# Performance work log

Hardware: AMD Instinct MI355X
Metric: run time of the kernel (lower is better)

The kernel has to match this reference:

```python
import jax, jax.numpy as jnp
import numpy as np


def conv2d(x, w, b, stride=1, pad=1):
    y = jax.lax.conv_general_dilated(
        x, w, (stride, stride), [(pad, pad), (pad, pad)],
        dimension_numbers=('NCHW', 'OIHW', 'NCHW'))
    return y + b[None, :, None, None]


def layernorm(x, g, b, eps=1e-5):
    mu = jnp.mean(x, -1, keepdims=True)
    var = jnp.mean((x - mu) ** 2, -1, keepdims=True)
    return (x - mu) * jax.lax.rsqrt(var + eps) * g + b


def setup_inputs() -> dict:
    key = jax.random.key(0)
    ks = iter(jax.random.split(key, 40))
    nf = 4

    def w(shape, scale=0.1):
        return (jax.random.normal(next(ks), shape, jnp.float32) * scale)

    inp = {}
    inp['x'] = jax.random.uniform(next(ks), (8, 3, 512, 512), jnp.float32)
    # curve-estimation convs (channel=4)
    inp['c1_w'], inp['c1_b'] = w((nf, 1, 3, 3)), w((nf,))
    inp['c2_w'], inp['c2_b'] = w((nf, nf, 3, 3)), w((nf,))
    inp['c3_w'], inp['c3_b'] = w((nf, nf, 3, 3)), w((nf,))
    inp['c4_w'], inp['c4_b'] = w((nf, nf, 3, 3)), w((nf,))
    inp['c5_w'], inp['c5_b'] = w((nf, 2 * nf, 3, 3)), w((nf,))
    inp['c6_w'], inp['c6_b'] = w((nf, 2 * nf, 3, 3)), w((nf,))
    inp['c7_w'], inp['c7_b'] = w((1, 2 * nf, 3, 3)), w((1,))
    # global branch: conv 1->16 stride 2, instance norm (affine)
    inp['m_w'], inp['m_b'] = w((16, 1, 3, 3)), w((16,))
    inp['in_g'] = jnp.ones((16,), jnp.float32)
    inp['in_b'] = jnp.zeros((16,), jnp.float32)
    # TF block (d_model=16, nhead=8, dim_ff=128), eval mode (no dropout)
    inp['attn_w'], inp['attn_b'] = w((48, 16)), w((48,))
    inp['out_w'], inp['out_b'] = w((16, 16)), w((16,))
    inp['l1_w'], inp['l1_b'] = w((128, 16)), w((128,))
    inp['l2_w'], inp['l2_b'] = w((16, 128)), w((16,))
    inp['n1_g'] = jnp.ones((16,), jnp.float32)
    inp['n1_b'] = jnp.zeros((16,), jnp.float32)
    inp['n2_g'] = jnp.ones((16,), jnp.float32)
    inp['n2_b'] = jnp.zeros((16,), jnp.float32)
    # F: Conv2d(16, 2, kernel=16, pad=0) over 16x16 -> [B,2,1,1]
    inp['f_w'], inp['f_b'] = w((2, 16, 16, 16)), w((2,))
    return inp


def _forward(x, c1_w, c1_b, c2_w, c2_b, c3_w, c3_b, c4_w, c4_b, c5_w, c5_b,
             c6_w, c6_b, c7_w, c7_b, m_w, m_b, in_g, in_b, attn_w, attn_b,
             out_w, out_b, l1_w, l1_b, l2_w, l2_b, n1_g, n1_b, n2_g, n2_b,
             f_w, f_b):
    relu = jax.nn.relu
    B, _, H, W = x.shape
    red, green, blue = x[:, 0:1], x[:, 1:2], x[:, 2:3]
    v = (red + green + blue) / 3.0  # [B,1,H,W]

    # curve-estimation branch
    x1 = relu(conv2d(v, c1_w, c1_b))
    x2 = relu(conv2d(x1, c2_w, c2_b))
    x3 = relu(conv2d(x2, c3_w, c3_b))
    x4 = relu(conv2d(x3, c4_w, c4_b))
    x5 = relu(conv2d(jnp.concatenate([x3, x4], 1), c5_w, c5_b))
    x6 = relu(conv2d(jnp.concatenate([x2, x5], 1), c6_w, c6_b))
    v_r = jax.nn.sigmoid(conv2d(jnp.concatenate([x1, x6], 1), c7_w, c7_b))

    # where(v>0.999999, 0.999999, .) ; where(v<1e-6, 1e-6, .)  == clip
    v0 = jnp.clip(v, 1e-6, 0.999999)

    # nearest-neighbor resize to 32x32 (torch 'nearest': floor(i * src/dst))
    idx_h = (jnp.arange(32) * H) // 32
    idx_w = (jnp.arange(32) * W) // 32
    v32 = v[:, :, idx_h][:, :, :, idx_w]  # [B,1,32,32]

    # model: conv stride2 -> leaky relu -> instance norm (affine)
    h = conv2d(v32, m_w, m_b, stride=2, pad=1)  # [B,16,16,16]
    h = jnp.where(h >= 0, h, 0.2 * h)
    mu = jnp.mean(h, (2, 3), keepdims=True)
    var = jnp.mean((h - mu) ** 2, (2, 3), keepdims=True)
    v1 = (h - mu) * jax.lax.rsqrt(var + 1e-5)
    v1 = v1 * in_g[None, :, None, None] + in_b[None, :, None, None]

    # TF block on [S=256, B, E=16] tokens, 8 heads of dim 2, eval mode
    bb, cc, ww, hh = v1.shape
    src = v1.reshape(bb, cc, ww * hh).transpose(2, 0, 1)  # [S,B,E]
    S, E, nH = ww * hh, cc, 8
    hd = E // nH
    qkv = src @ attn_w.T + attn_b  # [S,B,3E]
    q, k, vv = jnp.split(qkv, 3, axis=-1)
    q = q.reshape(S, bb, nH, hd)
    k = k.reshape(S, bb, nH, hd)
    vv = vv.reshape(S, bb, nH, hd)
    scores = jnp.einsum('sbhd,tbhd->bhst', q, k) / np.sqrt(hd).astype(np.float32)
    attn = jax.nn.softmax(scores, axis=-1)
    o = jnp.einsum('bhst,tbhd->sbhd', attn, vv).reshape(S, bb, E)
    o = o @ out_w.T + out_b
    src = layernorm(src + o, n1_g, n1_b)
    ff = jax.nn.relu(src @ l1_w.T + l1_b) @ l2_w.T + l2_b
    src = layernorm(src + ff, n2_g, n2_b)
    v5 = src.transpose(1, 2, 0).reshape(bb, cc, ww, hh)

    level = jax.nn.sigmoid(conv2d(v5, f_w, f_b, stride=1, pad=0))[:, :, 0, 0]  # [B,2]

    # per-sample exponent / threshold broadcast (vectorized .item() loop)
    g = (0.1 * level[:, 0] + 0.2)[:, None, None, None]   # [B,1,1,1]
    bcf = (0.04 * level[:, 1] + 0.06)[:, None, None, None]
    r0 = jnp.power(g, v_r)           # g ** r, elementwise per sample
    ev0 = jnp.power(v0, r0)
    L = 400.0 * (bcf - v) ** 3
    L = jnp.where(L < 1e-5, 1e-6, L)
    ev = ev0 - L
    vd = v + 1e-6
    enhance = jnp.concatenate([red / vd * ev, green / vd * ev, blue / vd * ev], 1)
    vvv = jnp.concatenate([v, v, v], 1)
    t = jnp.where(vvv > 0.04, jnp.zeros_like(enhance), enhance)
    return enhance, v_r, t


def reference(x, c1_w, c1_b, c2_w, c2_b, c3_w, c3_b, c4_w, c4_b, c5_w, c5_b,
              c6_w, c6_b, c7_w, c7_b, m_w, m_b, in_g, in_b, attn_w, attn_b,
              out_w, out_b, l1_w, l1_b, l2_w, l2_b, n1_g, n1_b, n2_g, n2_b,
              f_w, f_b):
    return _forward(x, c1_w, c1_b, c2_w, c2_b, c3_w, c3_b, c4_w, c4_b,
                    c5_w, c5_b, c6_w, c6_b, c7_w, c7_b, m_w, m_b, in_g, in_b,
                    attn_w, attn_b, out_w, out_b, l1_w, l1_b, l2_w, l2_b,
                    n1_g, n1_b, n2_g, n2_b, f_w, f_b)
```

## Files before the change

kernel.cpp:

```cpp
#include <hip/hip_runtime.h>
#include <math.h>

#define H 512
#define W 512
#define PLANE (H*W)
#define PLANE4 (PLANE/4)

typedef unsigned int uint;
typedef unsigned short ushort;
typedef _Float16 h2 __attribute__((ext_vector_type(2)));

__device__ __forceinline__ h2 bch2(uint u){ return __builtin_bit_cast(h2, u); }
__device__ __forceinline__ uint pkf16(float a, float b){
  return __builtin_bit_cast(uint, __builtin_amdgcn_cvt_pkrtz(a, b));
}

#define LOADWIN_EVEN(WIN, TL, S, YB, XB) { \
  _Pragma("unroll") for (int r_=0;r_<4;++r_){ \
    uint4 Ua = *(const uint4*)&(TL)[(((YB)+r_)*(S)+(XB))*4]; \
    uint4 Ub = *(const uint4*)&(TL)[(((YB)+r_)*(S)+(XB)+2)*4]; \
    WIN[r_][0][0]=bch2(Ua.x); WIN[r_][0][1]=bch2(Ua.y); \
    WIN[r_][1][0]=bch2(Ua.z); WIN[r_][1][1]=bch2(Ua.w); \
    WIN[r_][2][0]=bch2(Ub.x); WIN[r_][2][1]=bch2(Ub.y); \
    WIN[r_][3][0]=bch2(Ub.z); WIN[r_][3][1]=bch2(Ub.w); } }

#define LOADWIN_ODD(WIN, TL, S, YB, XB) { \
  _Pragma("unroll") for (int r_=0;r_<4;++r_){ \
    uint2 U0 = *(const uint2*)&(TL)[(((YB)+r_)*(S)+(XB))*4]; \
    uint4 U1 = *(const uint4*)&(TL)[(((YB)+r_)*(S)+(XB)+1)*4]; \
    uint2 U2 = *(const uint2*)&(TL)[(((YB)+r_)*(S)+(XB)+3)*4]; \
    WIN[r_][0][0]=bch2(U0.x); WIN[r_][0][1]=bch2(U0.y); \
    WIN[r_][1][0]=bch2(U1.x); WIN[r_][1][1]=bch2(U1.y); \
    WIN[r_][2][0]=bch2(U1.z); WIN[r_][2][1]=bch2(U1.w); \
    WIN[r_][3][0]=bch2(U2.x); WIN[r_][3][1]=bch2(U2.y); } }

#define LOADW(WL, OFF) uint WL[72]; \
  _Pragma("unroll") for (int i_=0;i_<72;++i_) WL[i_] = wpk[(OFF)+i_];

#define DOTACC2(WIN, WL) { \
  _Pragma("unroll") for (int p_=0;p_<2;++p_){ \
    _Pragma("unroll") for (int dy_=0;dy_<3;++dy_){ \
      _Pragma("unroll") for (int dx_=0;dx_<3;++dx_){ \
        h2 aa=WIN[dy_][dx_][p_],   bb=WIN[dy_][dx_+1][p_]; \
        h2 cc=WIN[dy_+1][dx_][p_], dd=WIN[dy_+1][dx_+1][p_]; \
        _Pragma("unroll") for (int co_=0;co_<4;++co_){ \
          h2 wv = bch2((WL)[(co_*2+p_)*9+dy_*3+dx_]); \
          a00[co_]=__builtin_amdgcn_fdot2(aa,wv,a00[co_],false); \
          a01[co_]=__builtin_amdgcn_fdot2(bb,wv,a01[co_],false); \
          a10[co_]=__builtin_amdgcn_fdot2(cc,wv,a10[co_],false); \
          a11[co_]=__builtin_amdgcn_fdot2(dd,wv,a11[co_],false); } } } } }

#define DOTACC1(WIN, WL, PBASE) { \
  _Pragma("unroll") for (int p_=0;p_<2;++p_){ \
    _Pragma("unroll") for (int dy_=0;dy_<3;++dy_){ \
      _Pragma("unroll") for (int dx_=0;dx_<3;++dx_){ \
        h2 wv = bch2((WL)[((PBASE)+p_)*9+dy_*3+dx_]); \
        s00=__builtin_amdgcn_fdot2(WIN[dy_][dx_][p_],  wv,s00,false); \
        s01=__builtin_amdgcn_fdot2(WIN[dy_][dx_+1][p_],wv,s01,false); \
        s10=__builtin_amdgcn_fdot2(WIN[dy_+1][dx_][p_],  wv,s10,false); \
        s11=__builtin_amdgcn_fdot2(WIN[dy_+1][dx_+1][p_],wv,s11,false); } } } }

#define STORE_CORE(TL, S, M00, M01, M10, M11) { \
    float v00[4],v01[4],v10[4],v11[4]; \
    _Pragma("unroll") \
    for (int co_=0;co_<4;++co_){ \
      v00[co_]=(M00)?fmaxf(a00[co_],0.f):0.f; \
      v01[co_]=(M01)?fmaxf(a01[co_],0.f):0.f; \
      v10[co_]=(M10)?fmaxf(a10[co_],0.f):0.f; \
      v11[co_]=(M11)?fmaxf(a11[co_],0.f):0.f; } \
    uint4 rowlo, rowhi; \
    rowlo.x=pkf16(v00[0],v00[1]); rowlo.y=pkf16(v00[2],v00[3]); \
    rowlo.z=pkf16(v01[0],v01[1]); rowlo.w=pkf16(v01[2],v01[3]); \
    rowhi.x=pkf16(v10[0],v10[1]); rowhi.y=pkf16(v10[2],v10[3]); \
    rowhi.z=pkf16(v11[0],v11[1]); rowhi.w=pkf16(v11[2],v11[3]); \
    *(uint4*)&(TL)[(y0*(S)+x0)*4]=rowlo; \
    *(uint4*)&(TL)[((y0+1)*(S)+x0)*4]=rowhi; }

#define STORE_TILE_B(TL, S, GOFF) { \
    bool okr0=(unsigned)(gy0+(GOFF)+y0  )<512u; \
    bool okr1=(unsigned)(gy0+(GOFF)+y0+1)<512u; \
    bool okc0=(unsigned)(gx0+(GOFF)+x0  )<512u; \
    bool okc1=(unsigned)(gx0+(GOFF)+x0+1)<512u; \
    STORE_CORE(TL, S, okr0&okc0, okr0&okc1, okr1&okc0, okr1&okc1) }

template<int S>
__device__ __forceinline__ void accp4sc(const ushort* __restrict__ pl,
    const float* __restrict__ w, int YB, int XB,
    float* a00, float* a01, float* a10, float* a11)
{
  float q[4][4];
  #pragma unroll
  for (int r=0;r<4;++r){
    const ushort* rp = pl + (YB+r)*S + XB;
    h2 p0 = bch2(*(const uint*)rp);
    h2 p1 = bch2(*(const uint*)(rp+2));
    q[r][0]=(float)p0.x; q[r][1]=(float)p0.y; q[r][2]=(float)p1.x; q[r][3]=(float)p1.y;
  }
  #pragma unroll
  for (int dy=0; dy<3; ++dy)
    #pragma unroll
    for (int dx=0; dx<3; ++dx){
      float q00=q[dy][dx], q01=q[dy][dx+1], q10=q[dy+1][dx], q11=q[dy+1][dx+1];
      #pragma unroll
      for (int co=0; co<4; ++co){
        float wv=w[co*9+dy*3+dx];
        a00[co]+=q00*wv; a01[co]+=q01*wv; a10[co]+=q10*wv; a11[co]+=q11*wv;
      }
    }
}

__launch_bounds__(256)
__global__ void k_mnorm(const float* __restrict__ xg, const float* __restrict__ mw,
                        const float* __restrict__ mb, const float* __restrict__ ing,
                        const float* __restrict__ inb, float* __restrict__ src,
                        const float* __restrict__ c2w, const float* __restrict__ c3w,
                        const float* __restrict__ c4w, const float* __restrict__ c5w,
                        const float* __restrict__ c6w, const float* __restrict__ c7w,
                        uint* __restrict__ wpk){
  if (blockIdx.x == 128){
    for (int i=threadIdx.x; i<540; i+=256){
      float f0, f1;
      if (i < 504){
        const float* sw; int CIB, rel;
        if      (i<72) { sw=c2w; CIB=0; rel=i;     int co=rel/18,p=(rel%18)/9,tap=rel%9;
                         f0=sw[(co*4+CIB+2*p)*9+tap]; f1=sw[(co*4+CIB+2*p+1)*9+tap]; }
        else if (i<144){ sw=c3w; CIB=0; rel=i-72;  int co=rel/18,p=(rel%18)/9,tap=rel%9;
                         f0=sw[(co*4+CIB+2*p)*9+tap]; f1=sw[(co*4+CIB+2*p+1)*9+tap]; }
        else if (i<216){ sw=c4w; CIB=0; rel=i-144; int co=rel/18,p=(rel%18)/9,tap=rel%9;
                         f0=sw[(co*4+CIB+2*p)*9+tap]; f1=sw[(co*4+CIB+2*p+1)*9+tap]; }
        else if (i<288){ sw=c5w; CIB=0; rel=i-216; int co=rel/18,p=(rel%18)/9,tap=rel%9;
                         f0=sw[(co*8+CIB+2*p)*9+tap]; f1=sw[(co*8+CIB+2*p+1)*9+tap]; }
        else if (i<360){ sw=c5w; CIB=4; rel=i-288; int co=rel/18,p=(rel%18)/9,tap=rel%9;
                         f0=sw[(co*8+CIB+2*p)*9+tap]; f1=sw[(co*8+CIB+2*p+1)*9+tap]; }
        else if (i<432){ sw=c6w; CIB=0; rel=i-360; int co=rel/18,p=(rel%18)/9,tap=rel%9;
                         f0=sw[(co*8+CIB+2*p)*9+tap]; f1=sw[(co*8+CIB+2*p+1)*9+tap]; }
        else           { sw=c6w; CIB=4; rel=i-432; int co=rel/18,p=(rel%18)/9,tap=rel%9;
                         f0=sw[(co*8+CIB+2*p)*9+tap]; f1=sw[(co*8+CIB+2*p+1)*9+tap]; }
      } else {
        int rel=i-504, p=rel/9, tap=rel%9;
        f0=c7w[(2*p)*9+tap]; f1=c7w[(2*p+1)*9+tap];
      }
      wpk[i] = pkf16(f0, f1);
    }
    return;
  }
  int bc = blockIdx.x;
  int b = bc >> 4, c = bc & 15;
  int tid = threadIdx.x;
  int i = tid >> 4, j = tid & 15;
  const float* xp = xg + (size_t)b*3*PLANE;
  float s = mb[c];
  #pragma unroll
  for (int dy=0; dy<3; ++dy){
    int ii = 2*i - 1 + dy;
    if ((unsigned)ii >= 32u) continue;
    #pragma unroll
    for (int dx=0; dx<3; ++dx){
      int jj = 2*j - 1 + dx;
      if ((unsigned)jj >= 32u) continue;
      int off = (ii*16)*W + jj*16;
      float vv = (xp[off] + xp[PLANE+off] + xp[2*PLANE+off]) * (1.f/3.f);
      s += vv * mw[c*9 + dy*3 + dx];
    }
  }
  float h = (s >= 0.f) ? s : 0.2f*s;
  __shared__ float red[256];
  red[tid] = h; __syncthreads();
  for (int off=128; off; off>>=1){ if (tid<off) red[tid]+=red[tid+off]; __syncthreads(); }
  float mu = red[0] * (1.f/256.f);
  __syncthreads();
  float d = h - mu;
  red[tid] = d*d; __syncthreads();
  for (int off=128; off; off>>=1){ if (tid<off) red[tid]+=red[tid+off]; __syncthreads(); }
  float var = red[0] * (1.f/256.f);
  float yv = d * rsqrtf(var + 1e-5f) * ing[c] + inb[c];
  src[(size_t)tid*128 + b*16 + c] = yv;
}

__launch_bounds__(256)
__global__ void k_attn2(const float* __restrict__ src, const float* __restrict__ aw,
                        const float* __restrict__ ab, float* __restrict__ obuf){
  int b = blockIdx.x >> 3, hh = blockIdx.x & 7;
  int t = threadIdx.x;
  __shared__ float kk0[256], kk1[256], vv0[256], vv1[256];
  int tok = t*8 + b;
  float s[16];
  #pragma unroll
  for (int e=0;e<16;++e) s[e] = src[tok*16+e];
  float q0=ab[2*hh], q1=ab[2*hh+1];
  float k0=ab[16+2*hh], k1=ab[16+2*hh+1];
  float v0=ab[32+2*hh], v1=ab[32+2*hh+1];
  #pragma unroll
  for (int e=0;e<16;++e){
    float sv=s[e];
    q0 += sv*aw[(2*hh  )*16+e]; q1 += sv*aw[(2*hh+1)*16+e];
    k0 += sv*aw[(16+2*hh)*16+e]; k1 += sv*aw[(16+2*hh+1)*16+e];
    v0 += sv*aw[(32+2*hh)*16+e]; v1 += sv*aw[(32+2*hh+1)*16+e];
  }
  kk0[t]=k0; kk1[t]=k1; vv0[t]=v0; vv1[t]=v1;
  __syncthreads();
  const float sc = 0.70710678118654752f;
  float l=0.f, a0=0.f, a1=0.f;
  for (int u=0;u<256;++u){
    float p = __expf((q0*kk0[u]+q1*kk1[u])*sc);
    l+=p; a0+=p*vv0[u]; a1+=p*vv1[u];
  }
  float inv=1.f/l;
  obuf[tok*16 + 2*hh]   = a0*inv;
  obuf[tok*16 + 2*hh+1] = a1*inv;
}

__launch_bounds__(256)
__global__ void k_post(const float* __restrict__ src, const float* __restrict__ obuf,
                       const float* __restrict__ ow, const float* __restrict__ ob,
                       const float* __restrict__ l1w, const float* __restrict__ l1b,
                       const float* __restrict__ l2w, const float* __restrict__ l2b,
                       const float* __restrict__ n1g, const float* __restrict__ n1b,
                       const float* __restrict__ n2g, const float* __restrict__ n2b,
                       const float* __restrict__ fw, const float* __restrict__ fb,
                       float* __restrict__ gb){
  __shared__ float srcl[256][17];
  __shared__ float red[512];
  int b = blockIdx.x, t = threadIdx.x;
  int tok = t*8 + b;
  float xv[16];
  {
    float orow[16], srow[16];
    #pragma unroll
    for (int e=0;e<16;++e){ orow[e]=obuf[tok*16+e]; srow[e]=src[tok*16+e]; }
    #pragma unroll
    for (int e=0;e<16;++e){
      float s2=ob[e];
      #pragma unroll
      for (int f=0;f<16;++f) s2 += orow[f]*ow[e*16+f];
      xv[e]=srow[e]+s2;
    }
    float mu=0.f;
    #pragma unroll
    for (int e=0;e<16;++e) mu+=xv[e];
    mu*=(1.f/16.f);
    float var=0.f;
    #pragma unroll
    for (int e=0;e<16;++e){ float d=xv[e]-mu; var+=d*d; }
    var*=(1.f/16.f);
    float rs=rsqrtf(var+1e-5f);
    #pragma unroll
    for (int e=0;e<16;++e) xv[e]=(xv[e]-mu)*rs*n1g[e]+n1b[e];
  }
  {
    float x2[16];
    #pragma unroll
    for (int e=0;e<16;++e) x2[e]=l2b[e];
    for (int ii=0;ii<128;++ii){
      float u=l1b[ii];
      #pragma unroll
      for (int e=0;e<16;++e) u += xv[e]*l1w[ii*16+e];
      u = fmaxf(u,0.f);
      #pragma unroll
      for (int e=0;e<16;++e) x2[e] += u*l2w[e*128+ii];
    }
    #pragma unroll
    for (int e=0;e<16;++e) x2[e]+=xv[e];
    float mu=0.f;
    #pragma unroll
    for (int e=0;e<16;++e) mu+=x2[e];
    mu*=(1.f/16.f);
    float var=0.f;
    #pragma unroll
    for (int e=0;e<16;++e){ float d=x2[e]-mu; var+=d*d; }
    var*=(1.f/16.f);
    float rs=rsqrtf(var+1e-5f);
    #pragma unroll
    for (int e=0;e<16;++e) srcl[t][e]=(x2[e]-mu)*rs*n2g[e]+n2b[e];
  }
  __syncthreads();
  {
    float p0=0.f,p1=0.f;
    #pragma unroll
    for (int c=0;c<16;++c){
      float sv=srcl[t][c];
      p0 += sv*fw[c*256+t];
      p1 += sv*fw[(16+c)*256+t];
    }
    red[t]=p0; red[256+t]=p1;
  }
  __syncthreads();
  for (int off=128; off; off>>=1){
    if (t<off){ red[t]+=red[t+off]; red[256+t]+=red[256+t+off]; }
    __syncthreads();
  }
  if (t==0){
    float lev0 = 1.f/(1.f+__expf(-(red[0]+fb[0])));
    float lev1 = 1.f/(1.f+__expf(-(red[256]+fb[1])));
    gb[b*2+0] = 0.1f*lev0+0.2f;
    gb[b*2+1] = 0.04f*lev1+0.06f;
  }
}

__launch_bounds__(512,2)
__global__ void k_megaconv(const float* __restrict__ xg,
    const float* __restrict__ c1w, const float* __restrict__ c1b,
    const float* __restrict__ c2b, const float* __restrict__ c3b,
    const float* __restrict__ c4b, const float* __restrict__ c5b,
    const float* __restrict__ c6b, const float* __restrict__ c7b,
    const uint* __restrict__ wpk, const float* __restrict__ gb2,
    float* __restrict__ out)
{
  __shared__ __align__(16) ushort vb[46*46];
  __shared__ __align__(16) ushort t1[44*44*4];
  __shared__ __align__(16) ushort t2[42*42*4];
  __shared__ __align__(16) ushort t3[40*40*4];
  __shared__ __align__(16) ushort t4[38*38*4];
  __shared__ __align__(16) ushort t5[36*36*4];
  __shared__ __align__(16) ushort t6[34*34*4];
  int wg=blockIdx.x, b=wg>>8, t=wg&255, ty=t>>4, tx=t&15;
  int gy0=ty*32, gx0=tx*32, tid=threadIdx.x;
  const float* xp = xg + (size_t)b*3*PLANE;
  const bool interior = (ty>=1)&(ty<=14)&(tx>=1)&(tx<=14);

  if (interior){
    for (int i=tid;i<46*46;i+=512){
      int rr=i/46, cc=i-rr*46;
      int off=(gy0-7+rr)*W + gx0-7+cc;
      float val=(xp[off]+xp[PLANE+off]+xp[2*PLANE+off])*(1.f/3.f);
      _Float16 hv=(_Float16)val;
      vb[i]=*(ushort*)&hv;
    }
  } else {
    for (int i=tid;i<46*46;i+=512){
      int rr=i/46, cc=i-rr*46;
      int gy=gy0-7+rr, gx=gx0-7+cc;
      float val=0.f;
      if (((unsigned)gy<512u)&((unsigned)gx<512u)){
        int off=gy*W+gx;
        val=(xp[off]+xp[PLANE+off]+xp[2*PLANE+off])*(1.f/3.f);
      }
      _Float16 hv=(_Float16)val;
      vb[i]=*(ushort*)&hv;
    }
  }
  __syncthreads();

  if (tid < 484){
    int qy=tid/22, qx=tid-qy*22, y0=2*qy, x0=2*qx;
    float a00[4],a01[4],a10[4],a11[4];
    #pragma unroll
    for (int co=0;co<4;++co){ float bv=c1b[co]; a00[co]=bv;a01[co]=bv;a10[co]=bv;a11[co]=bv; }
    accp4sc<46>(vb, c1w, y0, x0, a00,a01,a10,a11);
    if (interior){ STORE_CORE(t1, 44, true, true, true, true) }
    else         { STORE_TILE_B(t1, 44, -6) }
  }
  __syncthreads();

  if (tid < 441){
    int qy=tid/21, qx=tid-qy*21, y0=2*qy, x0=2*qx;
    float a00[4],a01[4],a10[4],a11[4];
    #pragma unroll
    for (int co=0;co<4;++co){ float bv=c2b[co]; a00[co]=bv;a01[co]=bv;a10[co]=bv;a11[co]=bv; }
    h2 win[4][4][2];
    LOADWIN_EVEN(win, t1, 44, y0, x0)
    LOADW(wl2, 0)
    DOTACC2(win, wl2)
    if (interior){ STORE_CORE(t2, 42, true, true, true, true) }
    else         { STORE_TILE_B(t2, 42, -5) }
  }
  __syncthreads();

  if (tid < 400){
    int qy=tid/20, qx=tid-qy*20, y0=2*qy, x0=2*qx;
    float a00[4],a01[4],a10[4],a11[4];
    #pragma unroll
    for (int co=0;co<4;++co){ float bv=c3b[co]; a00[co]=bv;a01[co]=bv;a10[co]=bv;a11[co]=bv; }
    h2 win[4][4][2];
    LOADWIN_EVEN(win, t2, 42, y0, x0)
    LOADW(wl3, 72)
    DOTACC2(win, wl3)
    if (interior){ STORE_CORE(t3, 40, true, true, true, true) }
    else         { STORE_TILE_B(t3, 40, -4) }
  }
  __syncthreads();

  if (tid < 361){
    int qy=tid/19, qx=tid-qy*19, y0=2*qy, x0=2*qx;
    float a00[4],a01[4],a10[4],a11[4];
    #pragma unroll
    for (int co=0;co<4;++co){ float bv=c4b[co]; a00[co]=bv;a01[co]=bv;a10[co]=bv;a11[co]=bv; }
    h2 win[4][4][2];
    LOADWIN_EVEN(win, t3, 40, y0, x0)
    LOADW(wl4, 144)
    DOTACC2(win, wl4)
    if (interior){ STORE_CORE(t4, 38, true, true, true, true) }
    else         { STORE_TILE_B(t4, 38, -3) }
  }
  __syncthreads();

  if (tid < 324){
    int qy=tid/18, qx=tid-qy*18, y0=2*qy, x0=2*qx;
    float a00[4],a01[4],a10[4],a11[4];
    #pragma unroll
    for (int co=0;co<4;++co){ float bv=c5b[co]; a00[co]=bv;a01[co]=bv;a10[co]=bv;a11[co]=bv; }
    {
      h2 win[4][4][2];
      LOADWIN_ODD(win, t3, 40, y0+1, x0+1)
      LOADW(wlA, 216)
      DOTACC2(win, wlA)
    }
    {
      h2 win[4][4][2];
      LOADWIN_EVEN(win, t4, 38, y0, x0)
      LOADW(wlB, 288)
      DOTACC2(win, wlB)
    }
    if (interior){ STORE_CORE(t5, 36, true, true, true, true) }
    else         { STORE_TILE_B(t5, 36, -2) }
  }
  __syncthreads();

  if (tid < 289){
    int qy=tid/17, qx=tid-qy*17, y0=2*qy, x0=2*qx;
    float a00[4],a01[4],a10[4],a11[4];
    #pragma unroll
    for (int co=0;co<4;++co){ float bv=c6b[co]; a00[co]=bv;a01[co]=bv;a10[co]=bv;a11[co]=bv; }
    {
      h2 win[4][4][2];
      LOADWIN_ODD(win, t2, 42, y0+3, x0+3)
      LOADW(wlA, 360)
      DOTACC2(win, wlA)
    }
    {
      h2 win[4][4][2];
      LOADWIN_EVEN(win, t5, 36, y0, x0)
      LOADW(wlB, 432)
      DOTACC2(win, wlB)
    }
    if (interior){ STORE_CORE(t6, 34, true, true, true, true) }
    else         { STORE_TILE_B(t6, 34, -1) }
  }
  __syncthreads();

  if (tid < 256){
    int qy=tid>>4, qx=tid&15, y0=2*qy, x0=2*qx;
    float bv=c7b[0];
    float s00=bv, s01=bv, s10=bv, s11=bv;
    uint wl7[36];
    #pragma unroll
    for (int i_=0;i_<36;++i_) wl7[i_]=wpk[504+i_];
    {
      h2 win[4][4][2];
      LOADWIN_ODD(win, t1, 44, y0+5, x0+5)
      DOTACC1(win, wl7, 0)
    }
    {
      h2 win[4][4][2];
      LOADWIN_EVEN(win, t6, 34, y0, x0)
      DOTACC1(win, wl7, 2)
    }
    s00 = 1.f/(1.f+__expf(-s00)); s01 = 1.f/(1.f+__expf(-s01));
    s10 = 1.f/(1.f+__expf(-s10)); s11 = 1.f/(1.f+__expf(-s11));
    float* vo = out + 6291456 + (size_t)b*PLANE;
    *(float2*)&vo[(gy0+y0  )*512 + gx0+x0] = make_float2(s00,s01);
    *(float2*)&vo[(gy0+y0+1)*512 + gx0+x0] = make_float2(s10,s11);

    float gg = gb2[b*2+0], bcf = gb2[b*2+1];
    float lg = log2f(gg);
    #pragma unroll
    for (int py=0; py<2; ++py){
      int gy=gy0+y0+py, gx=gx0+x0;
      int off=gy*W+gx;
      float2 R = *(const float2*)&xp[off];
      float2 G = *(const float2*)&xp[PLANE+off];
      float2 B = *(const float2*)&xp[2*PLANE+off];
      float vr0 = py? s10:s00, vr1 = py? s11:s01;
      float2 er,eg,eb,tr,tg,tb;
#define COMP1(RF,GF,BF,VRF,ER,EG,EB,TR,TG,TB) { \
      float vv=(RF+GF+BF)*(1.f/3.f); \
      float v0c=fminf(fmaxf(vv,1e-6f),0.999999f); \
      float r0=exp2f((VRF)*lg); \
      float ev0=exp2f(r0*log2f(v0c)); \
      float dd=bcf-vv; \
      float L=400.f*dd*dd*dd; \
      L=(L<1e-5f)?1e-6f:L; \
      float fac=(ev0-L)/(vv+1e-6f); \
      ER=RF*fac; EG=GF*fac; EB=BF*fac; \
      bool z=vv>0.04f; \
      TR=z?0.f:ER; TG=z?0.f:EG; TB=z?0.f:EB; }
      COMP1(R.x,G.x,B.x,vr0, er.x,eg.x,eb.x, tr.x,tg.x,tb.x)
      COMP1(R.y,G.y,B.y,vr1, er.y,eg.y,eb.y, tr.y,tg.y,tb.y)
#undef COMP1
      *(float2*)&out[(size_t)(b*3+0)*PLANE + off] = er;
      *(float2*)&out[(size_t)(b*3+1)*PLANE + off] = eg;
      *(float2*)&out[(size_t)(b*3+2)*PLANE + off] = eb;
      *(float2*)&out[8388608 + (size_t)(b*3+0)*PLANE + off] = tr;
      *(float2*)&out[8388608 + (size_t)(b*3+1)*PLANE + off] = tg;
      *(float2*)&out[8388608 + (size_t)(b*3+2)*PLANE + off] = tb;
    }
  }
}

extern "C" void kernel_launch(void* const* d_in, const int* in_sizes, int n_in,
                              void* d_out, int out_size, void* d_ws, size_t ws_size,
                              hipStream_t stream) {
  const float* x    = (const float*)d_in[0];
  const float* c1w  = (const float*)d_in[1];  const float* c1b = (const float*)d_in[2];
  const float* c2w  = (const float*)d_in[3];  const float* c2b = (const float*)d_in[4];
  const float* c3w  = (const float*)d_in[5];  const float* c3b = (const float*)d_in[6];
  const float* c4w  = (const float*)d_in[7];  const float* c4b = (const float*)d_in[8];
  const float* c5w  = (const float*)d_in[9];  const float* c5b = (const float*)d_in[10];
  const float* c6w  = (const float*)d_in[11]; const float* c6b = (const float*)d_in[12];
  const float* c7w  = (const float*)d_in[13]; const float* c7b = (const float*)d_in[14];
  const float* mw   = (const float*)d_in[15]; const float* mb  = (const float*)d_in[16];
  const float* ing  = (const float*)d_in[17]; const float* inb = (const float*)d_in[18];
  const float* aw   = (const float*)d_in[19]; const float* ab  = (const float*)d_in[20];
  const float* ow   = (const float*)d_in[21]; const float* ob  = (const float*)d_in[22];
  const float* l1w  = (const float*)d_in[23]; const float* l1b = (const float*)d_in[24];
  const float* l2w  = (const float*)d_in[25]; const float* l2b = (const float*)d_in[26];
  const float* n1g  = (const float*)d_in[27]; const float* n1b = (const float*)d_in[28];
  const float* n2g  = (const float*)d_in[29]; const float* n2b = (const float*)d_in[30];
  const float* fw   = (const float*)d_in[31]; const float* fb  = (const float*)d_in[32];

  uint* wpk = (uint*)d_ws;
  float* gb   = (float*)(wpk + 1024);
  float* src  = gb + 16;
  float* obuf = src + 32768;
  float* out  = (float*)d_out;

  k_mnorm<<<129,256,0,stream>>>(x, mw, mb, ing, inb, src,
                                c2w, c3w, c4w, c5w, c6w, c7w, wpk);
  k_attn2<<<64,256,0,stream>>>(src, aw, ab, obuf);
  k_post<<<8,256,0,stream>>>(src, obuf, ow, ob, l1w, l1b, l2w, l2b,
                             n1g, n1b, n2g, n2b, fw, fb, gb);
  k_megaconv<<<2048,512,0,stream>>>(x, c1w, c1b, c2b, c3b, c4b, c5b, c6b, c7b,
                                    wpk, gb, out);
}
```

Measured before the change: 184.1 us.

## Parallelize transformer post-processing per token with atomic accumulation into gate buffer

Result: faster. 153.7 us (median of 3 runs) (-16.5%).

```diff
diff --git a/kernel.cpp b/kernel.cpp
--- a/kernel.cpp
+++ b/kernel.cpp
@@ -116,8 +116,9 @@
                         const float* __restrict__ c2w, const float* __restrict__ c3w,
                         const float* __restrict__ c4w, const float* __restrict__ c5w,
                         const float* __restrict__ c6w, const float* __restrict__ c7w,
-                        uint* __restrict__ wpk){
+                        uint* __restrict__ wpk, float* __restrict__ gbacc){
   if (blockIdx.x == 128){
+    if (threadIdx.x < 16) gbacc[threadIdx.x] = 0.f;
     for (int i=threadIdx.x; i<540; i+=256){
       float f0, f1;
       if (i < 504){
@@ -210,90 +211,66 @@
   obuf[tok*16 + 2*hh+1] = a1*inv;
 }
 
-__launch_bounds__(256)
-__global__ void k_post(const float* __restrict__ src, const float* __restrict__ obuf,
-                       const float* __restrict__ ow, const float* __restrict__ ob,
-                       const float* __restrict__ l1w, const float* __restrict__ l1b,
-                       const float* __restrict__ l2w, const float* __restrict__ l2b,
-                       const float* __restrict__ n1g, const float* __restrict__ n1b,
-                       const float* __restrict__ n2g, const float* __restrict__ n2b,
-                       const float* __restrict__ fw, const float* __restrict__ fb,
-                       float* __restrict__ gb){
-  __shared__ float srcl[256][17];
-  __shared__ float red[512];
-  int b = blockIdx.x, t = threadIdx.x;
-  int tok = t*8 + b;
-  float xv[16];
-  {
-    float orow[16], srow[16];
-    #pragma unroll
-    for (int e=0;e<16;++e){ orow[e]=obuf[tok*16+e]; srow[e]=src[tok*16+e]; }
-    #pragma unroll
-    for (int e=0;e<16;++e){
-      float s2=ob[e];
-      #pragma unroll
-      for (int f=0;f<16;++f) s2 += orow[f]*ow[e*16+f];
-      xv[e]=srow[e]+s2;
-    }
+__launch_bounds__(64)
+__global__ void k_tok(const float* __restrict__ src, const float* __restrict__ obuf,
+                      const float* __restrict__ ow, const float* __restrict__ ob,
+                      const float* __restrict__ l1w, const float* __restrict__ l1b,
+                      const float* __restrict__ l2w, const float* __restrict__ l2b,
+                      const float* __restrict__ n1g, const float* __restrict__ n1b,
+                      const float* __restrict__ n2g, const float* __restrict__ n2b,
+                      const float* __restrict__ fw, float* __restrict__ gbacc){
+  int tok = blockIdx.x, tid = threadIdx.x;
+  int s = tok >> 3, b = tok & 7;
+  __shared__ float shx[16], shy[16], h1[128];
+  if (tid < 16){
+    float t2 = ob[tid];
+    #pragma unroll
+    for (int f=0;f<16;++f) t2 += obuf[tok*16+f]*ow[tid*16+f];
+    shx[tid] = src[tok*16+tid] + t2;
+  }
+  __syncthreads();
+  if (tid < 16){
     float mu=0.f;
     #pragma unroll
-    for (int e=0;e<16;++e) mu+=xv[e];
+    for (int e=0;e<16;++e) mu+=shx[e];
     mu*=(1.f/16.f);
     float var=0.f;
     #pragma unroll
-    for (int e=0;e<16;++e){ float d=xv[e]-mu; var+=d*d; }
+    for (int e=0;e<16;++e){ float d=shx[e]-mu; var+=d*d; }
     var*=(1.f/16.f);
-    float rs=rsqrtf(var+1e-5f);
-    #pragma unroll
-    for (int e=0;e<16;++e) xv[e]=(xv[e]-mu)*rs*n1g[e]+n1b[e];
-  }
-  {
-    float x2[16];
-    #pragma unroll
-    for (int e=0;e<16;++e) x2[e]=l2b[e];
-    for (int ii=0;ii<128;++ii){
-      float u=l1b[ii];
-      #pragma unroll
-      for (int e=0;e<16;++e) u += xv[e]*l1w[ii*16+e];
-      u = fmaxf(u,0.f);
-      #pragma unroll
-      for (int e=0;e<16;++e) x2[e] += u*l2w[e*128+ii];
-    }
-    #pragma unroll
-    for (int e=0;e<16;++e) x2[e]+=xv[e];
+    shy[tid] = (shx[tid]-mu)*rsqrtf(var+1e-5f)*n1g[tid]+n1b[tid];
+  }
+  __syncthreads();
+  for (int i=tid;i<128;i+=64){
+    float u=l1b[i];
+    #pragma unroll
+    for (int e=0;e<16;++e) u += shy[e]*l1w[i*16+e];
+    h1[i]=fmaxf(u,0.f);
+  }
+  __syncthreads();
+  if (tid < 16){
+    float x2=l2b[tid];
+    for (int jj=0;jj<128;++jj) x2 += h1[jj]*l2w[tid*128+jj];
+    shx[tid] = x2 + shy[tid];
+  }
+  __syncthreads();
+  if (tid < 16){
     float mu=0.f;
     #pragma unroll
-    for (int e=0;e<16;++e) mu+=x2[e];
+    for (int e=0;e<16;++e) mu+=shx[e];
     mu*=(1.f/16.f);
     float var=0.f;
     #pragma unroll
-    for (int e=0;e<16;++e){ float d=x2[e]-mu; var+=d*d; }
+    for (int e=0;e<16;++e){ float d=shx[e]-mu; var+=d*d; }
     var*=(1.f/16.f);
-    float rs=rsqrtf(var+1e-5f);
-    #pragma unroll
-    for (int e=0;e<16;++e) srcl[t][e]=(x2[e]-mu)*rs*n2g[e]+n2b[e];
-  }
-  __syncthreads();
-  {
-    float p0=0.f,p1=0.f;
-    #pragma unroll
-    for (int c=0;c<16;++c){
-      float sv=srcl[t][c];
-      p0 += sv*fw[c*256+t];
-      p1 += sv*fw[(16+c)*256+t];
-    }
-    red[t]=p0; red[256+t]=p1;
-  }
-  __syncthreads();
-  for (int off=128; off; off>>=1){
-    if (t<off){ red[t]+=red[t+off]; red[256+t]+=red[256+t+off]; }
-    __syncthreads();
-  }
-  if (t==0){
-    float lev0 = 1.f/(1.f+__expf(-(red[0]+fb[0])));
-    float lev1 = 1.f/(1.f+__expf(-(red[256]+fb[1])));
-    gb[b*2+0] = 0.1f*lev0+0.2f;
-    gb[b*2+1] = 0.04f*lev1+0.06f;
+    shy[tid]=(shx[tid]-mu)*rsqrtf(var+1e-5f)*n2g[tid]+n2b[tid];
+  }
+  __syncthreads();
+  if (tid < 2){
+    float p=0.f;
+    #pragma unroll
+    for (int c=0;c<16;++c) p += shy[c]*fw[(tid*16+c)*256 + s];
+    atomicAdd(&gbacc[b*2+tid], p);
   }
 }
 
@@ -303,7 +280,8 @@
     const float* __restrict__ c2b, const float* __restrict__ c3b,
     const float* __restrict__ c4b, const float* __restrict__ c5b,
     const float* __restrict__ c6b, const float* __restrict__ c7b,
-    const uint* __restrict__ wpk, const float* __restrict__ gb2,
+    const uint* __restrict__ wpk, const float* __restrict__ gbr,
+    const float* __restrict__ fb,
     float* __restrict__ out)
 {
   __shared__ __align__(16) ushort vb[46*46];
@@ -461,7 +439,10 @@
     *(float2*)&vo[(gy0+y0  )*512 + gx0+x0] = make_float2(s00,s01);
     *(float2*)&vo[(gy0+y0+1)*512 + gx0+x0] = make_float2(s10,s11);
 
-    float gg = gb2[b*2+0], bcf = gb2[b*2+1];
+    float lev0 = 1.f/(1.f+__expf(-(gbr[b*2+0]+fb[0])));
+    float lev1 = 1.f/(1.f+__expf(-(gbr[b*2+1]+fb[1])));
+    float gg  = 0.1f*lev0+0.2f;
+    float bcf = 0.04f*lev1+0.06f;
     float lg = log2f(gg);
     #pragma unroll
     for (int py=0; py<2; ++py){
@@ -519,16 +500,16 @@
   const float* fw   = (const float*)d_in[31]; const float* fb  = (const float*)d_in[32];
 
   uint* wpk = (uint*)d_ws;
-  float* gb   = (float*)(wpk + 1024);
-  float* src  = gb + 16;
+  float* gbacc = (float*)(wpk + 1024);
+  float* src  = gbacc + 16;
   float* obuf = src + 32768;
   float* out  = (float*)d_out;
 
   k_mnorm<<<129,256,0,stream>>>(x, mw, mb, ing, inb, src,
-                                c2w, c3w, c4w, c5w, c6w, c7w, wpk);
+                                c2w, c3w, c4w, c5w, c6w, c7w, wpk, gbacc);
   k_attn2<<<64,256,0,stream>>>(src, aw, ab, obuf);
-  k_post<<<8,256,0,stream>>>(src, obuf, ow, ob, l1w, l1b, l2w, l2b,
-                             n1g, n1b, n2g, n2b, fw, fb, gb);
+  k_tok<<<2048,64,0,stream>>>(src, obuf, ow, ob, l1w, l1b, l2w, l2b,
+                              n1g, n1b, n2g, n2b, fw, gbacc);
   k_megaconv<<<2048,512,0,stream>>>(x, c1w, c1b, c2b, c3b, c4b, c5b, c6b, c7b,
-                                    wpk, gb, out);
-}
+                                    wpk, gbacc, fb, out);
+}
```
